# Optimization experiments

Measured on AMD Instinct MI355X. Metric: run time of the kernel, lower is better.

The kernel has to match this reference:

```python
import jax, jax.numpy as jnp
import numpy as np

CHUNK = 400
L = 50          # encoder kernel and stride
JUMP = CHUNK // L  # 8 new frames per streaming step
N = 128         # encoder feature dim
B = 128         # bottleneck dim
H = 512         # TCN hidden dim
K = 3           # depthwise kernel size
R, X = 2, 7     # repeats x blocks, dilations 2^0..2^6
BUF = 516       # ring buffer length: JUMP + 2*sum(dilations)*R = 8 + 508
EPS = 1e-8


def setup_inputs() -> dict:
    key = jax.random.key(0)
    ks = jax.random.split(key, 16)
    nb = R * X
    w = lambda i, shape: jax.random.normal(ks[i], shape, jnp.float32) * 0.05
    return dict(
        mixture=jax.random.normal(ks[0], (1, 2, CHUNK), jnp.float32),
        encoder_buffer=jax.random.uniform(ks[1], (1, N, BUF), dtype=jnp.float32),
        layernorm_buffer=jax.random.normal(ks[2], (1, B, BUF), jnp.float32),
        W_enc=w(3, (N, 2, L)),              # encoder Conv1d(2->N, k=L, s=L)
        ln_g=jnp.ones((N,), jnp.float32),    # channelwise LayerNorm affine
        ln_b=jnp.zeros((N,), jnp.float32),
        W_bn=w(4, (B, N)),                   # bottleneck 1x1 conv
        blk_w1=w(5, (nb, H, B)),             # per-block pointwise in
        blk_p1=jnp.full((nb,), 0.25, jnp.float32),
        blk_g1=jnp.ones((nb, H), jnp.float32),
        blk_b1=jnp.zeros((nb, H), jnp.float32),
        blk_dw=w(6, (nb, H, K)),             # depthwise dilated conv
        blk_p2=jnp.full((nb,), 0.25, jnp.float32),
        blk_g2=jnp.ones((nb, H), jnp.float32),
        blk_b2=jnp.zeros((nb, H), jnp.float32),
        blk_w2=w(7, (nb, B, H)),             # per-block pointwise out
        W_mask=w(8, (N, B)),                 # mask 1x1 conv (C=1 source)
        W_dec=w(9, (L, N)),                  # decoder basis Linear(N->L)
    )


def _cln(x, g, b):
    # channelwise LayerNorm: normalize over channel dim per time frame. x: [1,C,T]
    mu = jnp.mean(x, axis=1, keepdims=True)
    var = jnp.var(x, axis=1, keepdims=True)
    return g[None, :, None] * (x - mu) * jax.lax.rsqrt(var + EPS) + b[None, :, None]


def _prelu(x, a):
    return jnp.where(x >= 0, x, a * x)


def _dwconv(x, w, d):
    # valid dilated depthwise conv. x: [1,H,T], w: [H,K] -> [1,H,T-(K-1)*d]
    return jax.lax.conv_general_dilated(
        x, w[:, None, :], window_strides=(1,), padding='VALID',
        rhs_dilation=(d,), feature_group_count=H,
        dimension_numbers=('NCH', 'OIH', 'NCH'))


def reference(mixture, encoder_buffer, layernorm_buffer, W_enc, ln_g, ln_b, W_bn,
              blk_w1, blk_p1, blk_g1, blk_b1, blk_dw, blk_p2, blk_g2, blk_b2,
              blk_w2, W_mask, W_dec):
    # --- encoder: Conv1d(2->N, k=L, s=L) + ReLU -> JUMP new frames, ring-shift buffer
    enc = jax.nn.relu(jax.lax.conv_general_dilated(
        mixture, W_enc, window_strides=(L,), padding='VALID',
        dimension_numbers=('NCH', 'OIH', 'NCH')))          # [1,N,JUMP]
    encoder_buffer = jnp.concatenate([encoder_buffer[:, :, JUMP:], enc], axis=2)

    # --- separator front-end (network[0:2]): cLN + bottleneck 1x1, per-frame causal
    ln_new = jnp.einsum('oc,bct->bot', W_bn, _cln(enc, ln_g, ln_b))  # [1,B,JUMP]
    layernorm_buffer = jnp.concatenate([layernorm_buffer[:, :, JUMP:], ln_new], axis=2)

    # --- TCN (network[2]): valid causal dilated blocks, each shrinks time by 2*d
    x = layernorm_buffer                                   # [1,B,516]
    for i in range(R * X):
        d = 2 ** (i % X)
        y = jnp.einsum('hc,bct->bht', blk_w1[i], x)
        y = _cln(_prelu(y, blk_p1[i]), blk_g1[i], blk_b1[i])
        y = _dwconv(y, blk_dw[i], d)                       # time -= (K-1)*d
        y = _cln(_prelu(y, blk_p2[i]), blk_g2[i], blk_b2[i])
        y = jnp.einsum('ch,bht->bct', blk_w2[i], y)
        x = x[:, :, (K - 1) * d:] + y                      # residual on trailing frames
    # x: [1,B,JUMP]

    # --- mask conv (network[3]) + ReLU, reshape to [1,C=1,N,JUMP]
    mask = jax.nn.relu(jnp.einsum('nc,bct->bnt', W_mask, x)).reshape(1, 1, N, JUMP)

    # --- decoder: mask the newest JUMP encoder frames, basis Linear(N->L), stride=L
    src_w = encoder_buffer[:, None, :, -JUMP:] * mask      # [1,1,N,JUMP]
    est_source = jnp.einsum('ln,bcnt->bctl', W_dec, src_w).reshape(1, 1, JUMP * L)
    return est_source, encoder_buffer, layernorm_buffer
```

## Files before the change

kernel.cpp:

```cpp
#include <hip/hip_runtime.h>

#define CHUNK 400
#define LWIN 50
#define JUMP 8
#define NCH 128
#define BCH 128
#define HCH 512
#define NBLK 14
#define BUF 516
#define SHIFT 508
#define EPSV 1e-8f
#define NWG 136
#define NGRP 8
#define GSIZE 17

__device__ __forceinline__ void cstore(float* p, float v) {
    __hip_atomic_store(p, v, __ATOMIC_RELAXED, __HIP_MEMORY_SCOPE_AGENT);
}

__device__ __forceinline__ void gsync(unsigned* bar, int slot, int tid, int wg) {
    __syncthreads();
    if (tid == 0) {
        unsigned* base = bar + slot * (9 * 32);
        unsigned* loc  = base + (wg & 7) * 32;
        unsigned* root = base + 8 * 32;
        unsigned prev = __hip_atomic_fetch_add(loc, 1u, __ATOMIC_RELAXED,
                                               __HIP_MEMORY_SCOPE_AGENT);
        if (prev == GSIZE - 1)
            __hip_atomic_fetch_add(root, 1u, __ATOMIC_RELAXED,
                                   __HIP_MEMORY_SCOPE_AGENT);
        while (__hip_atomic_load(root, __ATOMIC_RELAXED, __HIP_MEMORY_SCOPE_AGENT) < NGRP)
            __builtin_amdgcn_s_sleep(2);
        (void)__hip_atomic_load(root, __ATOMIC_ACQUIRE, __HIP_MEMORY_SCOPE_AGENT);
    }
    __syncthreads();
}

__device__ __forceinline__ void fwait(unsigned* flp, int base, int cnt, int tid) {
    if (tid < cnt) {
        unsigned* p = flp + base + tid;
        while (__hip_atomic_load(p, __ATOMIC_RELAXED, __HIP_MEMORY_SCOPE_AGENT) == 0)
            __builtin_amdgcn_s_sleep(1);
    }
    __syncthreads();
}
__device__ __forceinline__ void fset(unsigned* flp, int idx, int tid) {
    __syncthreads();
    if (tid == 0)
        __hip_atomic_store(flp + idx, 1u, __ATOMIC_RELAXED, __HIP_MEMORY_SCOPE_AGENT);
}

__device__ __forceinline__ void stage1_core(
    int tid, int lane, int wid, int t0, int nf,
    const float* __restrict__ w1b, float aPr,
    const float* __restrict__ gv, const float* __restrict__ bv,
    float* __restrict__ yout, float* redf, float* statsf, const float* xsv)
{
    float acc[4] = {0.f, 0.f, 0.f, 0.f};
    const float4* __restrict__ wr = (const float4*)(w1b + (size_t)tid * BCH);
    const float4* __restrict__ xv = (const float4*)xsv;
    #pragma unroll 4
    for (int c4 = 0; c4 < 32; ++c4) {
        float4 w = wr[c4];
        #pragma unroll
        for (int f = 0; f < 4; ++f) {
            float4 x = xv[f * 32 + c4];
            acc[f] += w.x * x.x + w.y * x.y + w.z * x.z + w.w * x.w;
        }
    }
    #pragma unroll
    for (int f = 0; f < 4; ++f) acc[f] = acc[f] >= 0.f ? acc[f] : aPr * acc[f];
    for (int f = 0; f < nf; ++f) {
        float s = acc[f], q = acc[f] * acc[f];
        #pragma unroll
        for (int o = 32; o; o >>= 1) { s += __shfl_xor(s, o); q += __shfl_xor(q, o); }
        if (lane == 0) { redf[(wid * 4 + f) * 2] = s; redf[(wid * 4 + f) * 2 + 1] = q; }
    }
    __syncthreads();
    if (tid < nf) {
        float s = 0.f, q = 0.f;
        #pragma unroll
        for (int w = 0; w < 8; ++w) { s += redf[(w * 4 + tid) * 2]; q += redf[(w * 4 + tid) * 2 + 1]; }
        float mean = s * (1.f / HCH);
        float var = q * (1.f / HCH) - mean * mean;
        statsf[tid * 2] = mean; statsf[tid * 2 + 1] = rsqrtf(var + EPSV);
    }
    __syncthreads();
    float gg = gv[tid], bb = bv[tid];
    for (int f = 0; f < nf; ++f)
        cstore(&yout[(t0 + f) * HCH + tid],
               gg * (acc[f] - statsf[f * 2]) * statsf[f * 2 + 1] + bb);
}

__global__ __launch_bounds__(512) void k_fused(
    const float* __restrict__ mixture, const float* __restrict__ inEnc,
    const float* __restrict__ inLn, const float* __restrict__ Wenc,
    const float* __restrict__ lng, const float* __restrict__ lnb,
    const float* __restrict__ Wbn, const float* __restrict__ w1,
    const float* __restrict__ p1, const float* __restrict__ g1,
    const float* __restrict__ b1, const float* __restrict__ dwc,
    const float* __restrict__ p2, const float* __restrict__ g2,
    const float* __restrict__ b2, const float* __restrict__ w2,
    const float* __restrict__ Wmask, const float* __restrict__ Wdec,
    float* __restrict__ est, float* __restrict__ outEnc, float* __restrict__ outLn,
    unsigned* __restrict__ fl, float* __restrict__ enc,
    float* __restrict__ xbuf, float* __restrict__ ybuf,
    int nx, int ny, int mode)
{
    __shared__ float xs[4 * BCH];
    __shared__ float ys[4 * 528];
    __shared__ float redf[8 * 4 * 2];
    __shared__ float statsf[4 * 2];

    const int wg = blockIdx.x;
    const int tid = threadIdx.x;
    const int lane = tid & 63, wid = tid >> 6;
    const int j = wg;

    if (wg < 8) {
        int t = wg;
        float e = 0.f;
        if (tid < 128) {
            int c = tid;
            const float* w = Wenc + c * 100;
            const float* m = mixture + t * LWIN;
            #pragma unroll 10
            for (int l = 0; l < LWIN; ++l) e += m[l] * w[l] + m[CHUNK + l] * w[LWIN + l];
            e = fmaxf(e, 0.f);
            cstore(&enc[t * NCH + c], e);
            outEnc[c * BUF + SHIFT + t] = e;
            float s = e, q = e * e;
            #pragma unroll
            for (int o = 32; o; o >>= 1) { s += __shfl_xor(s, o); q += __shfl_xor(q, o); }
            if (lane == 0) { redf[(wid * 4) * 2] = s; redf[(wid * 4) * 2 + 1] = q; }
        }
        __syncthreads();
        if (tid < 128) {
            float S = redf[0] + redf[8], Q = redf[1] + redf[9];
            float mean = S * (1.f / NCH);
            float var = Q * (1.f / NCH) - mean * mean;
            float r = rsqrtf(var + EPSV);
            xs[tid] = lng[tid] * (e - mean) * r + lnb[tid];
        }
        __syncthreads();
        if (tid < 128) {
            float acc = 0.f;
            const float4* wr = (const float4*)(Wbn + tid * NCH);
            const float4* nv = (const float4*)xs;
            #pragma unroll 8
            for (int j4 = 0; j4 < 32; ++j4) {
                float4 w = wr[j4]; float4 x = nv[j4];
                acc += w.x * x.x + w.y * x.y + w.z * x.z + w.w * x.w;
            }
            outLn[tid * BUF + SHIFT + t] = acc;
            cstore(&xbuf[(SHIFT + t) * BCH + tid], acc);
        }
    } else {
        int ch = wg - 8;
        for (int t = tid; t < SHIFT; t += 512)
            outEnc[ch * BUF + t] = inEnc[ch * BUF + t + JUMP];
        if (ch < 127) {
            int f = tid >> 7, c = tid & 127;
            int t = 4 * ch + f;
            float v = inLn[c * BUF + t + JUMP];
            cstore(&xbuf[t * BCH + c], v);
            outLn[c * BUF + t] = v;
        }
    }
    if (mode == 0) fset(fl, 0 * NWG + wg, tid); else gsync(fl, 0, tid, wg);

    if (4 * j < BUF) {
        if (mode == 0) {
            int base, cnt;
            if (j <= 126)      { base = 8 + j; cnt = 1; }
            else if (j == 127) { base = 0;     cnt = 4; }
            else               { base = 4;     cnt = 4; }
            fwait(fl, base, cnt, tid);
        }
        int t0 = 4 * j;
        int nf = min(4, BUF - t0);
        for (int idx = tid; idx < nf * BCH; idx += 512) xs[idx] = xbuf[t0 * BCH + idx];
        __syncthreads();
        stage1_core(tid, lane, wid, t0, nf, w1, p1[0], g1, b1, ybuf, redf, statsf, xs);
    }
    if (mode == 0) fset(fl, 1 * NWG + wg, tid); else gsync(fl, 1, tid, wg);

    const float* xin = xbuf;
    int T = BUF;
    for (int i = 0; i < NBLK; ++i) {
        float* xout = xbuf + (size_t)((i + 1) % nx) * (BUF * BCH);
        const float* ycur = ybuf + (size_t)(i % ny) * (BUF * HCH);
        float* ynext = ybuf + (size_t)((i + 1) % ny) * (BUF * HCH);
        int d = 1 << (i % 7);
        int Tout = T - 2 * d;
        int t0 = 4 * j;
        if (t0 < Tout) {
            if (mode == 0) {
                int jmaxe = (T - 1) >> 2;
                int jmax = min(j + ((3 + 2 * d) >> 2), jmaxe);
                fwait(fl + (1 + i) * NWG, j, jmax - j + 1, tid);
                if (i == NBLK - 1) fwait(fl, 4 * j, 4, tid);
            }
            int nf = min(4, Tout - t0);
            const float* dwb = dwc + (size_t)i * HCH * 3;
            float d0 = dwb[tid * 3], d1 = dwb[tid * 3 + 1], d2 = dwb[tid * 3 + 2];
            float a2 = p2[i];
            float y[4];
            for (int f = 0; f < nf; ++f) {
                int t = t0 + f;
                float v = d0 * ycur[t * HCH + tid] + d1 * ycur[(t + d) * HCH + tid]
                        + d2 * ycur[(t + 2 * d) * HCH + tid];
                y[f] = v >= 0.f ? v : a2 * v;
            }
            for (int f = 0; f < nf; ++f) {
                float s = y[f], q = y[f] * y[f];
                #pragma unroll
                for (int o = 32; o; o >>= 1) { s += __shfl_xor(s, o); q += __shfl_xor(q, o); }
                if (lane == 0) { redf[(wid * 4 + f) * 2] = s; redf[(wid * 4 + f) * 2 + 1] = q; }
            }
            __syncthreads();
            if (tid < nf) {
                float s = 0.f, q = 0.f;
                #pragma unroll
                for (int w = 0; w < 8; ++w) { s += redf[(w * 4 + tid) * 2]; q += redf[(w * 4 + tid) * 2 + 1]; }
                float mean = s * (1.f / HCH);
                float var = q * (1.f / HCH) - mean * mean;
                statsf[tid * 2] = mean; statsf[tid * 2 + 1] = rsqrtf(var + EPSV);
            }
            __syncthreads();
            {
                float gg = g2[i * HCH + tid], bb = b2[i * HCH + tid];
                int pidx = (tid >> 7) * 132 + (tid & 127);
                for (int f = 0; f < nf; ++f)
                    ys[f * 528 + pidx] = gg * (y[f] - statsf[f * 2]) * statsf[f * 2 + 1] + bb;
            }
            __syncthreads();
            int c = tid >> 2, p = tid & 3;
            float acc[4] = {0.f, 0.f, 0.f, 0.f};
            const float4* wr = (const float4*)(w2 + (size_t)i * BCH * HCH + c * HCH + p * 128);
            const float* yb = ys + p * 132;
            #pragma unroll 4
            for (int j4 = 0; j4 < 32; ++j4) {
                float4 w = wr[j4];
                #pragma unroll
                for (int f = 0; f < 4; ++f) {
                    float4 x = *(const float4*)&yb[f * 528 + j4 * 4];
                    acc[f] += w.x * x.x + w.y * x.y + w.z * x.z + w.w * x.w;
                }
            }
            for (int f = 0; f < nf; ++f) {
                acc[f] += __shfl_xor(acc[f], 1);
                acc[f] += __shfl_xor(acc[f], 2);
            }
            if (p == 0) {
                for (int f = 0; f < nf; ++f) {
                    int t = t0 + f;
                    float xv = xin[(t + 2 * d) * BCH + c] + acc[f];
                    cstore(&xout[t * BCH + c], xv);
                    xs[f * BCH + c] = xv;
                }
            }
            __syncthreads();
            if (i < NBLK - 1) {
                stage1_core(tid, lane, wid, t0, nf,
                            w1 + (size_t)(i + 1) * HCH * BCH, p1[i + 1],
                            g1 + (i + 1) * HCH, b1 + (i + 1) * HCH, ynext, redf, statsf, xs);
            } else {
                int cc = tid & 127, f = tid >> 7;
                float m = 0.f;
                const float4* wm = (const float4*)(Wmask + cc * BCH);
                const float4* xv = (const float4*)(xs + f * BCH);
                #pragma unroll 8
                for (int j4 = 0; j4 < 32; ++j4) {
                    float4 w = wm[j4]; float4 x = xv[j4];
                    m += w.x * x.x + w.y * x.y + w.z * x.z + w.w * x.w;
                }
                m = fmaxf(m, 0.f);
                ys[f * BCH + cc] = m * enc[(t0 + f) * NCH + cc];
                __syncthreads();
                if (tid < 4 * LWIN) {
                    int ff = tid / LWIN, l = tid % LWIN;
                    float e = 0.f;
                    const float4* wd = (const float4*)(Wdec + l * NCH);
                    const float4* sv = (const float4*)(ys + ff * BCH);
                    #pragma unroll 8
                    for (int j4 = 0; j4 < 32; ++j4) {
                        float4 w = wd[j4]; float4 x = sv[j4];
                        e += w.x * x.x + w.y * x.y + w.z * x.z + w.w * x.w;
                    }
                    est[(t0 + ff) * LWIN + l] = e;
                }
            }
        }
        if (mode == 0) fset(fl, (2 + i) * NWG + wg, tid);
        else if (i < NBLK - 1) gsync(fl, 2 + i, tid, wg);
        T = Tout;
        xin = xout;
    }
}

extern "C" void kernel_launch(void* const* d_in, const int* in_sizes, int n_in,
                              void* d_out, int out_size, void* d_ws, size_t ws_size,
                              hipStream_t stream) {
    const float* mixture = (const float*)d_in[0];
    const float* inEnc   = (const float*)d_in[1];
    const float* inLn    = (const float*)d_in[2];
    const float* Wenc    = (const float*)d_in[3];
    const float* lng     = (const float*)d_in[4];
    const float* lnb     = (const float*)d_in[5];
    const float* Wbn     = (const float*)d_in[6];
    const float* w1      = (const float*)d_in[7];
    const float* p1      = (const float*)d_in[8];
    const float* g1      = (const float*)d_in[9];
    const float* b1      = (const float*)d_in[10];
    const float* dwc     = (const float*)d_in[11];
    const float* p2      = (const float*)d_in[12];
    const float* g2      = (const float*)d_in[13];
    const float* b2      = (const float*)d_in[14];
    const float* w2      = (const float*)d_in[15];
    const float* Wmask   = (const float*)d_in[16];
    const float* Wdec    = (const float*)d_in[17];

    float* est    = (float*)d_out;
    float* outEnc = est + CHUNK;
    float* outLn  = outEnc + NCH * BUF;

    unsigned* fl = (unsigned*)d_ws;
    float* enc  = (float*)d_ws + 4608;
    float* xbuf = enc + 1024;
    const size_t xstr = (size_t)BUF * BCH;
    const size_t ystr = (size_t)BUF * HCH;

    int nx, ny, mode;
    size_t need_fresh = (4608 + 1024 + 15 * xstr + 14 * ystr) * 4ull;
    if (ws_size >= need_fresh) { nx = 15; ny = 14; mode = 0; }
    else                       { nx = 2;  ny = 2;  mode = 1; }
    float* ybuf = xbuf + (size_t)nx * xstr;

    hipMemsetAsync(d_ws, 0, 18432, stream);

    void* args[] = { &mixture, &inEnc, &inLn, &Wenc, &lng, &lnb, &Wbn, &w1, &p1,
                     &g1, &b1, &dwc, &p2, &g2, &b2, &w2, &Wmask, &Wdec,
                     &est, &outEnc, &outLn, &fl, &enc, &xbuf, &ybuf,
                     &nx, &ny, &mode };
    hipLaunchCooperativeKernel((const void*)k_fused, dim3(NWG), dim3(512),
                               (void**)args, 0, stream);
}
```

Baseline: 377.8 us.

## Use double-buffered activations with flag dataflow, dropping the barrier fallback

Removes the hierarchical grid-barrier fallback and always uses per-workgroup flag dataflow. The per-block x and y buffers shrink from 15/14 fresh copies to two ping-pong copies each, so the working set is far smaller and more cache-resident. To stay safe under buffer reuse, each workgroup also waits on flags from earlier neighbours (jlo) so that no reader of the previous block still needs the data, and loads of shared buffers become relaxed atomic loads. In exchange there are wider flag waits, which add dependency stalls, and the atomic loads may cost more than plain loads.

```diff
diff --git a/kernel.cpp b/kernel.cpp
--- a/kernel.cpp
+++ b/kernel.cpp
@@ -11,29 +11,12 @@
 #define SHIFT 508
 #define EPSV 1e-8f
 #define NWG 136
-#define NGRP 8
-#define GSIZE 17
 
 __device__ __forceinline__ void cstore(float* p, float v) {
     __hip_atomic_store(p, v, __ATOMIC_RELAXED, __HIP_MEMORY_SCOPE_AGENT);
 }
-
-__device__ __forceinline__ void gsync(unsigned* bar, int slot, int tid, int wg) {
-    __syncthreads();
-    if (tid == 0) {
-        unsigned* base = bar + slot * (9 * 32);
-        unsigned* loc  = base + (wg & 7) * 32;
-        unsigned* root = base + 8 * 32;
-        unsigned prev = __hip_atomic_fetch_add(loc, 1u, __ATOMIC_RELAXED,
-                                               __HIP_MEMORY_SCOPE_AGENT);
-        if (prev == GSIZE - 1)
-            __hip_atomic_fetch_add(root, 1u, __ATOMIC_RELAXED,
-                                   __HIP_MEMORY_SCOPE_AGENT);
-        while (__hip_atomic_load(root, __ATOMIC_RELAXED, __HIP_MEMORY_SCOPE_AGENT) < NGRP)
-            __builtin_amdgcn_s_sleep(2);
-        (void)__hip_atomic_load(root, __ATOMIC_ACQUIRE, __HIP_MEMORY_SCOPE_AGENT);
-    }
-    __syncthreads();
+__device__ __forceinline__ float cload(const float* p) {
+    return __hip_atomic_load(p, __ATOMIC_RELAXED, __HIP_MEMORY_SCOPE_AGENT);
 }
 
 __device__ __forceinline__ void fwait(unsigned* flp, int base, int cnt, int tid) {
@@ -104,8 +87,7 @@
     const float* __restrict__ Wmask, const float* __restrict__ Wdec,
     float* __restrict__ est, float* __restrict__ outEnc, float* __restrict__ outLn,
     unsigned* __restrict__ fl, float* __restrict__ enc,
-    float* __restrict__ xbuf, float* __restrict__ ybuf,
-    int nx, int ny, int mode)
+    float* __restrict__ xbuf, float* __restrict__ ybuf)
 {
     __shared__ float xs[4 * BCH];
     __shared__ float ys[4 * 528];
@@ -116,6 +98,8 @@
     const int tid = threadIdx.x;
     const int lane = tid & 63, wid = tid >> 6;
     const int j = wg;
+    const size_t xstr = (size_t)BUF * BCH;
+    const size_t ystr = (size_t)BUF * HCH;
 
     if (wg < 8) {
         int t = wg;
@@ -167,40 +151,38 @@
             outLn[c * BUF + t] = v;
         }
     }
-    if (mode == 0) fset(fl, 0 * NWG + wg, tid); else gsync(fl, 0, tid, wg);
+    fset(fl, 0 * NWG + wg, tid);
 
     if (4 * j < BUF) {
-        if (mode == 0) {
-            int base, cnt;
-            if (j <= 126)      { base = 8 + j; cnt = 1; }
-            else if (j == 127) { base = 0;     cnt = 4; }
-            else               { base = 4;     cnt = 4; }
-            fwait(fl, base, cnt, tid);
-        }
+        int base, cnt;
+        if (j <= 126)      { base = 8 + j; cnt = 1; }
+        else if (j == 127) { base = 0;     cnt = 4; }
+        else               { base = 4;     cnt = 4; }
+        fwait(fl, base, cnt, tid);
         int t0 = 4 * j;
         int nf = min(4, BUF - t0);
-        for (int idx = tid; idx < nf * BCH; idx += 512) xs[idx] = xbuf[t0 * BCH + idx];
+        for (int idx = tid; idx < nf * BCH; idx += 512) xs[idx] = cload(&xbuf[t0 * BCH + idx]);
         __syncthreads();
         stage1_core(tid, lane, wid, t0, nf, w1, p1[0], g1, b1, ybuf, redf, statsf, xs);
     }
-    if (mode == 0) fset(fl, 1 * NWG + wg, tid); else gsync(fl, 1, tid, wg);
-
-    const float* xin = xbuf;
+    fset(fl, 1 * NWG + wg, tid);
+
     int T = BUF;
     for (int i = 0; i < NBLK; ++i) {
-        float* xout = xbuf + (size_t)((i + 1) % nx) * (BUF * BCH);
-        const float* ycur = ybuf + (size_t)(i % ny) * (BUF * HCH);
-        float* ynext = ybuf + (size_t)((i + 1) % ny) * (BUF * HCH);
+        const float* xin = xbuf + (size_t)(i & 1) * xstr;
+        float* xout      = xbuf + (size_t)((i + 1) & 1) * xstr;
+        const float* ycur = ybuf + (size_t)(i & 1) * ystr;
+        float* ynext      = ybuf + (size_t)((i + 1) & 1) * ystr;
         int d = 1 << (i % 7);
         int Tout = T - 2 * d;
         int t0 = 4 * j;
         if (t0 < Tout) {
-            if (mode == 0) {
-                int jmaxe = (T - 1) >> 2;
-                int jmax = min(j + ((3 + 2 * d) >> 2), jmaxe);
-                fwait(fl + (1 + i) * NWG, j, jmax - j + 1, tid);
-                if (i == NBLK - 1) fwait(fl, 4 * j, 4, tid);
-            }
+            int jmaxe = (T - 1) >> 2;
+            int jmax = min(j + ((3 + 2 * d) >> 2), jmaxe);
+            int woff = (i >= 1 && i < NBLK - 1) ? ((3 + 2 * (1 << ((i - 1) % 7))) >> 2) : 0;
+            int jlo = max(0, j - woff);
+            fwait(fl + (1 + i) * NWG, jlo, jmax - jlo + 1, tid);
+            if (i == NBLK - 1) fwait(fl, 4 * j, 4, tid);
             int nf = min(4, Tout - t0);
             const float* dwb = dwc + (size_t)i * HCH * 3;
             float d0 = dwb[tid * 3], d1 = dwb[tid * 3 + 1], d2 = dwb[tid * 3 + 2];
@@ -208,8 +190,9 @@
             float y[4];
             for (int f = 0; f < nf; ++f) {
                 int t = t0 + f;
-                float v = d0 * ycur[t * HCH + tid] + d1 * ycur[(t + d) * HCH + tid]
-                        + d2 * ycur[(t + 2 * d) * HCH + tid];
+                float v = d0 * cload(&ycur[t * HCH + tid])
+                        + d1 * cload(&ycur[(t + d) * HCH + tid])
+                        + d2 * cload(&ycur[(t + 2 * d) * HCH + tid]);
                 y[f] = v >= 0.f ? v : a2 * v;
             }
             for (int f = 0; f < nf; ++f) {
@@ -255,7 +238,7 @@
             if (p == 0) {
                 for (int f = 0; f < nf; ++f) {
                     int t = t0 + f;
-                    float xv = xin[(t + 2 * d) * BCH + c] + acc[f];
+                    float xv = cload(&xin[(t + 2 * d) * BCH + c]) + acc[f];
                     cstore(&xout[t * BCH + c], xv);
                     xs[f * BCH + c] = xv;
                 }
@@ -276,7 +259,7 @@
                     m += w.x * x.x + w.y * x.y + w.z * x.z + w.w * x.w;
                 }
                 m = fmaxf(m, 0.f);
-                ys[f * BCH + cc] = m * enc[(t0 + f) * NCH + cc];
+                ys[f * BCH + cc] = m * cload(&enc[(t0 + f) * NCH + cc]);
                 __syncthreads();
                 if (tid < 4 * LWIN) {
                     int ff = tid / LWIN, l = tid % LWIN;
@@ -292,10 +275,8 @@
                 }
             }
         }
-        if (mode == 0) fset(fl, (2 + i) * NWG + wg, tid);
-        else if (i < NBLK - 1) gsync(fl, 2 + i, tid, wg);
+        fset(fl, (2 + i) * NWG + wg, tid);
         T = Tout;
-        xin = xout;
     }
 }
 
@@ -326,23 +307,15 @@
     float* outLn  = outEnc + NCH * BUF;
 
     unsigned* fl = (unsigned*)d_ws;
-    float* enc  = (float*)d_ws + 4608;
+    float* enc  = (float*)d_ws + 2304;
     float* xbuf = enc + 1024;
-    const size_t xstr = (size_t)BUF * BCH;
-    const size_t ystr = (size_t)BUF * HCH;
-
-    int nx, ny, mode;
-    size_t need_fresh = (4608 + 1024 + 15 * xstr + 14 * ystr) * 4ull;
-    if (ws_size >= need_fresh) { nx = 15; ny = 14; mode = 0; }
-    else                       { nx = 2;  ny = 2;  mode = 1; }
-    float* ybuf = xbuf + (size_t)nx * xstr;
-
-    hipMemsetAsync(d_ws, 0, 18432, stream);
+    float* ybuf = xbuf + 2 * (size_t)BUF * BCH;
+
+    hipMemsetAsync(d_ws, 0, 9216, stream);
 
     void* args[] = { &mixture, &inEnc, &inLn, &Wenc, &lng, &lnb, &Wbn, &w1, &p1,
                      &g1, &b1, &dwc, &p2, &g2, &b2, &w2, &Wmask, &Wdec,
-                     &est, &outEnc, &outLn, &fl, &enc, &xbuf, &ybuf,
-                     &nx, &ny, &mode };
+                     &est, &outEnc, &outLn, &fl, &enc, &xbuf, &ybuf };
     hipLaunchCooperativeKernel((const void*)k_fused, dim3(NWG), dim3(512),
                                (void**)args, 0, stream);
 }
```

After: 379.5 us. No clear change (+0.5%).
